# Kernel optimization log

Hardware: AMD Instinct MI355X
Metric: run time of the kernel (lower is better)

## Reference

```python
import jax, jax.numpy as jnp
import numpy as np
from math import log2, ceil

HEADS = 16
BLOCK = 16
EPS = 1e-8


def flip_every_two(t):
    # flip adjacent pairs along axis 1: (B, n, ...) with n even
    B, n = t.shape[0], t.shape[1]
    rest = t.shape[2:]
    t = t.reshape(B, n // 2, 2, *rest)
    t = jnp.flip(t, axis=2)
    return t.reshape(B, n, *rest)


def masked_aggregate(t, mask, average=True):
    # t: (B, n, 2, d), mask: (B, n, 2) bool; aggregate over axis=2
    m = mask[..., None]
    s = jnp.where(m, t, 0.0).sum(axis=2)
    total = mask.sum(axis=2)  # (B, n) int
    if average:
        s = s / jnp.clip(total, 1)[..., None].astype(t.dtype)
    return jnp.where((total == 0)[..., None], 0.0, s)


def _forward(x, Wq, bq, Wk, bk, Wv, bv, mask):
    b, n, hidden = x.shape
    h, bsz, d = HEADS, BLOCK, hidden // HEADS
    scale = d ** -0.5
    pad_to_len = 2 ** ceil(log2(n))
    pad = pad_to_len - n
    if pad != 0:
        x = jnp.pad(x, ((0, 0), (0, pad), (0, 0)))
        mask = jnp.pad(mask, ((0, 0), (0, pad)), constant_values=False)
    N = pad_to_len

    def split_heads(t):  # (b, N, h*d) -> (b*h, N, d)
        return t.reshape(b, N, h, d).transpose(0, 2, 1, 3).reshape(b * h, N, d)

    q = split_heads(x @ Wq + bq) * scale
    k = split_heads(x @ Wk + bk)
    v = split_heads(x @ Wv + bv)
    m = jnp.broadcast_to(mask[:, None, :], (b, h, N)).reshape(b * h, N)

    num_levels = int(log2(N // bsz)) - 2
    qkvs = [(q, k, v, m)]
    for _ in range(num_levels):
        B, L, _ = q.shape
        q2 = q.reshape(B, L // 2, 2, d)
        k2 = k.reshape(B, L // 2, 2, d)
        v2 = v.reshape(B, L // 2, 2, d)
        m2 = m.reshape(B, L // 2, 2)
        q = masked_aggregate(q2, m2, average=True)
        k = masked_aggregate(k2, m2, average=True)
        v = masked_aggregate(v2, m2, average=False)
        m = jnp.any(m2, axis=2)
        qkvs.append((q, k, v, m))
    qkvs = [qkvs[0]] + qkvs

    Ys = []
    for ind, (ql, kl, vl, ml) in enumerate(reversed(qkvs)):
        is_last = ind == len(qkvs) - 1
        B, L, _ = ql.shape
        nb = L // bsz
        qb = ql.reshape(B, nb, bsz, d)
        kb = kl.reshape(B, nb, bsz, d)
        vb = vl.reshape(B, nb, bsz, d)
        mb = ml.reshape(B, nb, bsz)
        k_mask = mb if is_last else flip_every_two(mb)
        S_mask = mb[..., :, None] & k_mask[..., None, :]  # (B, nb, bsz, bsz)
        if not is_last:
            kb = flip_every_two(kb)
            vb = flip_every_two(vb)
        S = jnp.einsum('bnid,bnjd->bnij', qb, kb)
        S = jnp.where(S_mask, S, jnp.finfo(S.dtype).min)
        S = S - S.max(axis=-1, keepdims=True)
        A = jnp.exp(S)
        Y = jnp.einsum('bnij,bnjd->bnid', A, vb)
        Ys.append((Y.reshape(B, L, d), A.sum(axis=-1).reshape(B, L)))

    Y, A = Ys[0]
    for ind in range(1, len(Ys)):
        is_last = ind == len(Ys) - 1
        if not is_last:
            Y = jnp.repeat(Y, 2, axis=1)
            A = jnp.repeat(A, 2, axis=1)
        Y = Ys[ind][0] + Y
        A = Ys[ind][1] + A

    out = Y / (A + EPS)[..., None]  # (b*h, N, d)
    out = out.reshape(b, h, N, d).transpose(0, 2, 1, 3).reshape(b, N, hidden)
    return out[:, :n]


def setup_inputs():
    key = jax.random.key(0)
    ks = jax.random.split(key, 7)
    b, n, hidden = 2, 8192, 1024
    s = 1.0 / np.sqrt(hidden)
    x = jax.random.normal(ks[0], (b, n, hidden), jnp.float32)
    mask = jnp.ones((b, n), dtype=bool)
    Wq = jax.random.normal(ks[1], (hidden, hidden), jnp.float32) * s
    Wk = jax.random.normal(ks[2], (hidden, hidden), jnp.float32) * s
    Wv = jax.random.normal(ks[3], (hidden, hidden), jnp.float32) * s
    bq = jax.random.normal(ks[4], (hidden,), jnp.float32) * 0.01
    bk = jax.random.normal(ks[5], (hidden,), jnp.float32) * 0.01
    bv = jax.random.normal(ks[6], (hidden,), jnp.float32) * 0.01
    return {"x": x, "mask": mask, "Wq": Wq, "bq": bq, "Wk": Wk, "bk": bk, "Wv": Wv, "bv": bv}


def reference(x, mask, Wq, bq, Wk, bk, Wv, bv):
    return _forward(x, Wq, bq, Wk, bk, Wv, bv, mask)
```

## Files before the change

### kernel.cpp

```cpp
#include <hip/hip_runtime.h>
#include <hip/hip_bf16.h>

typedef __attribute__((ext_vector_type(4))) float f32x4;
typedef __attribute__((ext_vector_type(8))) __bf16 bf16x8;
typedef __attribute__((ext_vector_type(4))) unsigned int u32x4;

#define TE 33423360ull

__device__ __forceinline__ unsigned short f2b_rne(float f) {
  unsigned u = __float_as_uint(f);
  return (unsigned short)((u + 0x7fffu + ((u >> 16) & 1u)) >> 16);
}
__device__ __forceinline__ float b2f(unsigned s) { return __uint_as_float(s << 16); }

__device__ __forceinline__ void gload_lds16(const unsigned short* g, unsigned short* l) {
  __builtin_amdgcn_global_load_lds((const __attribute__((address_space(1))) void*)g,
                                   (__attribute__((address_space(3))) void*)l, 16, 0, 0);
}

__global__ void conv_x(const float* __restrict__ x, unsigned short* __restrict__ xb) {
  size_t i = ((size_t)blockIdx.x * 256 + threadIdx.x) * 8;
  f32x4 A = *(const f32x4*)(x + i);
  f32x4 B = *(const f32x4*)(x + i + 4);
  u32x4 o;
  o[0] = f2b_rne(A[0]) | ((unsigned)f2b_rne(A[1]) << 16);
  o[1] = f2b_rne(A[2]) | ((unsigned)f2b_rne(A[3]) << 16);
  o[2] = f2b_rne(B[0]) | ((unsigned)f2b_rne(B[1]) << 16);
  o[3] = f2b_rne(B[2]) | ((unsigned)f2b_rne(B[3]) << 16);
  *(u32x4*)(xb + i) = o;
}

__global__ void transpose_w(const float* __restrict__ Wq, const float* __restrict__ Wk,
                            const float* __restrict__ Wv, unsigned short* __restrict__ wt) {
  int z = blockIdx.z;
  const float* W = (z == 0) ? Wq : (z == 1) ? Wk : Wv;
  __shared__ float t[32][33];
  int n0 = blockIdx.x * 32, k0 = blockIdx.y * 32;
  int tx = threadIdx.x, ty = threadIdx.y;
#pragma unroll
  for (int j = 0; j < 4; ++j)
    t[ty + j * 8][tx] = W[(size_t)(k0 + ty + j * 8) * 1024 + n0 + tx];
  __syncthreads();
  unsigned short* o = wt + (size_t)z * 1048576;
#pragma unroll
  for (int j = 0; j < 4; ++j)
    o[(size_t)(n0 + ty + j * 8) * 1024 + k0 + tx] = f2b_rne(t[tx][ty + j * 8]);
}

__global__ __launch_bounds__(256) void gemm_qkv(
    const unsigned short* __restrict__ xb, const unsigned short* __restrict__ wt,
    const float* __restrict__ bq, const float* __restrict__ bk, const float* __restrict__ bv,
    unsigned short* __restrict__ qkv) {
  int z = blockIdx.z;
  const unsigned short* w = wt + (size_t)z * 1048576;
  int flat = blockIdx.y * 8 + blockIdx.x;
  int swz = (flat & 7) * 128 + (flat >> 3);
  int m0 = (swz >> 3) * 128, n0 = (swz & 7) * 128;
  __shared__ unsigned short At[8192];
  __shared__ unsigned short Bt[8192];
  int tid = threadIdx.x;
  int lane = tid & 63, wid = tid >> 6;
  int g = lane >> 4, r16 = lane & 15;
  int wm = (wid >> 1) * 64, wn = (wid & 1) * 64;
  int srow = wid * 8 + (lane >> 3);
  int scol = ((lane & 7) ^ (lane >> 3)) * 8;
  f32x4 zero4 = {0.f, 0.f, 0.f, 0.f};
  f32x4 acc[4][4];
#pragma unroll
  for (int i = 0; i < 4; ++i)
#pragma unroll
    for (int j = 0; j < 4; ++j) acc[i][j] = zero4;

  for (int kt = 0; kt < 16; ++kt) {
#pragma unroll
    for (int c = 0; c < 4; ++c) {
      const unsigned short* ga = xb + (size_t)(m0 + c * 32 + srow) * 1024 + kt * 64 + scol;
      gload_lds16(ga, At + c * 2048 + wid * 512);
    }
#pragma unroll
    for (int c = 0; c < 4; ++c) {
      const unsigned short* gb = w + (size_t)(n0 + c * 32 + srow) * 1024 + kt * 64 + scol;
      gload_lds16(gb, Bt + c * 2048 + wid * 512);
    }
    __syncthreads();
#pragma unroll
    for (int kk = 0; kk < 2; ++kk) {
      bf16x8 af[4], bf_[4];
#pragma unroll
      for (int t = 0; t < 4; ++t) {
        int m = wm + t * 16 + r16;
        af[t] = *(const bf16x8*)((const char*)At + m * 128 + (((kk * 4 + g) ^ (m & 7)) * 16));
        int n = wn + t * 16 + r16;
        bf_[t] = *(const bf16x8*)((const char*)Bt + n * 128 + (((kk * 4 + g) ^ (n & 7)) * 16));
      }
#pragma unroll
      for (int i = 0; i < 4; ++i)
#pragma unroll
        for (int j = 0; j < 4; ++j)
          acc[i][j] = __builtin_amdgcn_mfma_f32_16x16x32_bf16(af[i], bf_[j], acc[i][j], 0, 0, 0);
    }
    __syncthreads();
  }
  const float* bias = (z == 0) ? bq : (z == 1) ? bk : bv;
  float scale = (z == 0) ? 0.125f : 1.0f;
  unsigned short* outp = qkv + (size_t)z * TE;
#pragma unroll
  for (int i = 0; i < 4; ++i) {
#pragma unroll
    for (int j = 0; j < 4; ++j) {
      int col = n0 + wn + j * 16 + r16;
      float bc = bias[col];
#pragma unroll
      for (int r = 0; r < 4; ++r) {
        int row = m0 + wm + i * 16 + g * 4 + r;
        float val = (acc[i][j][r] + bc) * scale;
        int bh = ((row >> 13) << 4) + (col >> 6);
        int pos = row & 8191;
        int dd = col & 63;
        outp[((size_t)bh * 8192 + pos) * 64 + dd] = f2b_rne(val);
      }
    }
  }
}

__global__ __launch_bounds__(256) void agg_all(unsigned short* __restrict__ qkv) {
  int seg = blockIdx.x, bh = blockIdx.y, z = blockIdx.z;
  unsigned short* tb = qkv + (size_t)z * TE;
  __shared__ unsigned short b0[16384];
  __shared__ unsigned short b1[8192];
  int t = threadIdx.x;
  const unsigned short* ip = tb + ((size_t)bh * 8192 + (size_t)seg * 256) * 64;
#pragma unroll
  for (int j = 0; j < 8; ++j)
    *(u32x4*)(b0 + (j * 256 + t) * 8) = *(const u32x4*)(ip + (size_t)(j * 256 + t) * 8);
  __syncthreads();
  float sc = (z < 2) ? 0.5f : 1.0f;
  long off = 8192;
  unsigned short* src = b0;
  unsigned short* dst = b1;
  for (int l = 1; l <= 7; ++l) {
    int R = 256 >> l;
    int chunks = R * 32;
    for (int c = t; c < chunks; c += 256) {
      int r = c >> 5, cc = c & 31;
      unsigned a = *(const unsigned*)(src + (2 * r) * 64 + cc * 2);
      unsigned b = *(const unsigned*)(src + (2 * r + 1) * 64 + cc * 2);
      float lo = (b2f(a & 0xffffu) + b2f(b & 0xffffu)) * sc;
      float hi = (b2f(a >> 16) + b2f(b >> 16)) * sc;
      unsigned o = f2b_rne(lo) | ((unsigned)f2b_rne(hi) << 16);
      *(unsigned*)(dst + r * 64 + cc * 2) = o;
      unsigned short* op =
          tb + (size_t)off * 2048 + ((size_t)bh * (8192 >> l) + (size_t)seg * R + r) * 64;
      *(unsigned*)(op + cc * 2) = o;
    }
    __syncthreads();
    off += 8192 >> l;
    unsigned short* tmp = src; src = dst; dst = tmp;
  }
}

union U8 { bf16x8 v; unsigned short u[8]; };

__device__ __forceinline__ void attn_unit(
    const unsigned short* kb, const unsigned short* vb, bf16x8 qf0, bf16x8 qf1,
    int g, int qr, f32x4 (&acc)[4], float& aacc) {
  bf16x8 kf0 = *(const bf16x8*)(kb + qr * 64 + g * 8);
  bf16x8 kf1 = *(const bf16x8*)(kb + qr * 64 + 32 + g * 8);
  f32x4 s = {0.f, 0.f, 0.f, 0.f};
  s = __builtin_amdgcn_mfma_f32_16x16x32_bf16(kf0, qf0, s, 0, 0, 0);
  s = __builtin_amdgcn_mfma_f32_16x16x32_bf16(kf1, qf1, s, 0, 0, 0);
  float mx = fmaxf(fmaxf(s[0], s[1]), fmaxf(s[2], s[3]));
  mx = fmaxf(mx, __shfl_xor(mx, 16));
  mx = fmaxf(mx, __shfl_xor(mx, 32));
  float av[4], asum = 0.f;
#pragma unroll
  for (int r = 0; r < 4; ++r) { av[r] = __expf(s[r] - mx); asum += av[r]; }
  asum += __shfl_xor(asum, 16);
  asum += __shfl_xor(asum, 32);
  aacc += asum;
  U8 A_;
#pragma unroll
  for (int r = 0; r < 4; ++r) A_.u[r] = f2b_rne(av[r]);
#pragma unroll
  for (int r = 4; r < 8; ++r) A_.u[r] = 0;
#pragma unroll
  for (int cg = 0; cg < 4; ++cg) {
    int c = cg * 16 + qr;
    U8 B_;
#pragma unroll
    for (int r = 0; r < 4; ++r) B_.u[r] = vb[(g * 4 + r) * 64 + c];
#pragma unroll
    for (int r = 4; r < 8; ++r) B_.u[r] = 0;
    acc[cg] = __builtin_amdgcn_mfma_f32_16x16x32_bf16(A_.v, B_.v, acc[cg], 0, 0, 0);
  }
}

__global__ __launch_bounds__(64) void attn_fused(const unsigned short* __restrict__ qkv,
                                                 float* __restrict__ outp) {
  int flat = blockIdx.y * 512 + blockIdx.x;
  int fb = (flat & 7) * 2048 + (flat >> 3);
  int bh = fb >> 9, B0 = fb & 511;
  int lane = threadIdx.x;
  int g = lane >> 4, qr = lane & 15;
  const unsigned short* qt = qkv;
  const unsigned short* kt = qkv + TE;
  const unsigned short* vt = qkv + 2 * TE;
  f32x4 acc[4];
#pragma unroll
  for (int cg = 0; cg < 4; ++cg) acc[cg] = (f32x4){0.f, 0.f, 0.f, 0.f};
  float aacc = 0.f;
  int off = 0;
#pragma unroll
  for (int l = 0; l <= 7; ++l) {
    int L = 8192 >> l;
    size_t base = (size_t)off * 2048 + (size_t)bh * L * 64;
    const unsigned short* qb = qt + base;
    const unsigned short* kb = kt + base;
    const unsigned short* vb = vt + base;
    int qrow = (B0 * 16 + qr) >> l;
    bf16x8 qf0 = *(const bf16x8*)(qb + (size_t)qrow * 64 + g * 8);
    bf16x8 qf1 = *(const bf16x8*)(qb + (size_t)qrow * 64 + 32 + g * 8);
    int P = B0 >> l;
    if (l == 0) {
      attn_unit(kb + (size_t)P * 1024, vb + (size_t)P * 1024, qf0, qf1, g, qr, acc, aacc);
      attn_unit(kb + (size_t)(P ^ 1) * 1024, vb + (size_t)(P ^ 1) * 1024, qf0, qf1, g, qr, acc, aacc);
    } else {
      int S_ = P ^ 1;
      attn_unit(kb + (size_t)S_ * 1024, vb + (size_t)S_ * 1024, qf0, qf1, g, qr, acc, aacc);
    }
    off += L;
  }
  int b_ = bh >> 4, h_ = bh & 15;
#pragma unroll
  for (int r = 0; r < 4; ++r) {
    int p = g * 4 + r;
    float ap = __shfl(aacc, p);
    float inv = 1.0f / (ap + 1e-8f);
    float* od = outp + ((size_t)(b_ * 8192 + B0 * 16 + p)) * 1024 + h_ * 64 + qr;
#pragma unroll
    for (int cg = 0; cg < 4; ++cg) od[cg * 16] = acc[cg][r] * inv;
  }
}

extern "C" void kernel_launch(void* const* d_in, const int* in_sizes, int n_in,
                              void* d_out, int out_size, void* d_ws, size_t ws_size,
                              hipStream_t stream) {
  const float* x = (const float*)d_in[0];
  const float* Wq = (const float*)d_in[2];
  const float* bq = (const float*)d_in[3];
  const float* Wk = (const float*)d_in[4];
  const float* bk = (const float*)d_in[5];
  const float* Wv = (const float*)d_in[6];
  const float* bv = (const float*)d_in[7];
  float* out = (float*)d_out;

  char* ws = (char*)d_ws;
  size_t o = 0;
  unsigned short* qkv = (unsigned short*)(ws + o); o += 200540160ull;
  unsigned short* wt = (unsigned short*)(ws + o); o += 6291456ull;
  unsigned short* xb = (unsigned short*)(ws + o); o += 33554432ull;
  if (ws_size < o) return;

  conv_x<<<8192, 256, 0, stream>>>(x, xb);
  transpose_w<<<dim3(32, 32, 3), dim3(32, 8), 0, stream>>>(Wq, Wk, Wv, wt);
  gemm_qkv<<<dim3(8, 128, 3), 256, 0, stream>>>(xb, wt, bq, bk, bv, qkv);
  agg_all<<<dim3(32, 32, 3), 256, 0, stream>>>(qkv);
  attn_fused<<<dim3(512, 32), 64, 0, stream>>>(qkv, out);
}
```

Before: 259.6 us.

## Double-buffer QKV GEMM LDS tiles and stage epilogue through LDS for vector stores

Splits the GEMM's shared memory into two buffers so the next K-tile's global-to-LDS loads are issued before computing on the current tile, overlapping memory latency with MFMA work. The epilogue now writes bf16 results into a padded LDS tile and then emits 16-byte vectorized row stores to the head-split output layout, replacing scattered 2-byte stores. This doubles LDS usage (64KB per block), which may reduce occupancy.

```diff
diff --git a/kernel.cpp b/kernel.cpp
--- a/kernel.cpp
+++ b/kernel.cpp
@@ -56,14 +56,26 @@
   int flat = blockIdx.y * 8 + blockIdx.x;
   int swz = (flat & 7) * 128 + (flat >> 3);
   int m0 = (swz >> 3) * 128, n0 = (swz & 7) * 128;
-  __shared__ unsigned short At[8192];
-  __shared__ unsigned short Bt[8192];
+  __shared__ unsigned short lds[32768];
   int tid = threadIdx.x;
   int lane = tid & 63, wid = tid >> 6;
   int g = lane >> 4, r16 = lane & 15;
   int wm = (wid >> 1) * 64, wn = (wid & 1) * 64;
   int srow = wid * 8 + (lane >> 3);
   int scol = ((lane & 7) ^ (lane >> 3)) * 8;
+
+  auto stage = [&](int b, int kt) {
+    unsigned short* Ab = lds + b * 16384;
+    unsigned short* Bb = Ab + 8192;
+#pragma unroll
+    for (int c = 0; c < 4; ++c) {
+      gload_lds16(xb + (size_t)(m0 + c * 32 + srow) * 1024 + kt * 64 + scol,
+                  Ab + c * 2048 + wid * 512);
+      gload_lds16(w + (size_t)(n0 + c * 32 + srow) * 1024 + kt * 64 + scol,
+                  Bb + c * 2048 + wid * 512);
+    }
+  };
+
   f32x4 zero4 = {0.f, 0.f, 0.f, 0.f};
   f32x4 acc[4][4];
 #pragma unroll
@@ -71,27 +83,22 @@
 #pragma unroll
     for (int j = 0; j < 4; ++j) acc[i][j] = zero4;
 
+  stage(0, 0);
+  __syncthreads();
   for (int kt = 0; kt < 16; ++kt) {
-#pragma unroll
-    for (int c = 0; c < 4; ++c) {
-      const unsigned short* ga = xb + (size_t)(m0 + c * 32 + srow) * 1024 + kt * 64 + scol;
-      gload_lds16(ga, At + c * 2048 + wid * 512);
-    }
-#pragma unroll
-    for (int c = 0; c < 4; ++c) {
-      const unsigned short* gb = w + (size_t)(n0 + c * 32 + srow) * 1024 + kt * 64 + scol;
-      gload_lds16(gb, Bt + c * 2048 + wid * 512);
-    }
-    __syncthreads();
+    int cb = kt & 1;
+    if (kt < 15) stage(cb ^ 1, kt + 1);
+    const char* Ab = (const char*)(lds + cb * 16384);
+    const char* Bb = Ab + 16384;
 #pragma unroll
     for (int kk = 0; kk < 2; ++kk) {
       bf16x8 af[4], bf_[4];
 #pragma unroll
       for (int t = 0; t < 4; ++t) {
         int m = wm + t * 16 + r16;
-        af[t] = *(const bf16x8*)((const char*)At + m * 128 + (((kk * 4 + g) ^ (m & 7)) * 16));
+        af[t] = *(const bf16x8*)(Ab + m * 128 + (((kk * 4 + g) ^ (m & 7)) * 16));
         int n = wn + t * 16 + r16;
-        bf_[t] = *(const bf16x8*)((const char*)Bt + n * 128 + (((kk * 4 + g) ^ (n & 7)) * 16));
+        bf_[t] = *(const bf16x8*)(Bb + n * 128 + (((kk * 4 + g) ^ (n & 7)) * 16));
       }
 #pragma unroll
       for (int i = 0; i < 4; ++i)
@@ -101,26 +108,31 @@
     }
     __syncthreads();
   }
+
   const float* bias = (z == 0) ? bq : (z == 1) ? bk : bv;
   float scale = (z == 0) ? 0.125f : 1.0f;
-  unsigned short* outp = qkv + (size_t)z * TE;
+  unsigned short* Ct = lds;
 #pragma unroll
   for (int i = 0; i < 4; ++i) {
 #pragma unroll
     for (int j = 0; j < 4; ++j) {
-      int col = n0 + wn + j * 16 + r16;
-      float bc = bias[col];
+      int col = wn + j * 16 + r16;
+      float bc = bias[n0 + col];
 #pragma unroll
       for (int r = 0; r < 4; ++r) {
-        int row = m0 + wm + i * 16 + g * 4 + r;
-        float val = (acc[i][j][r] + bc) * scale;
-        int bh = ((row >> 13) << 4) + (col >> 6);
-        int pos = row & 8191;
-        int dd = col & 63;
-        outp[((size_t)bh * 8192 + pos) * 64 + dd] = f2b_rne(val);
+        int row = wm + i * 16 + g * 4 + r;
+        Ct[row * 136 + col] = f2b_rne((acc[i][j][r] + bc) * scale);
       }
     }
   }
+  __syncthreads();
+  int rr = tid >> 1, hc = (tid & 1) * 64;
+  int R = m0 + rr, Cb = n0 + hc;
+  int bh = ((R >> 13) << 4) + (Cb >> 6);
+  unsigned short* outp = qkv + (size_t)z * TE + ((size_t)bh * 8192 + (size_t)(R & 8191)) * 64;
+#pragma unroll
+  for (int ch = 0; ch < 8; ++ch)
+    *(u32x4*)(outp + ch * 8) = *(const u32x4*)(Ct + rr * 136 + hc + ch * 8);
 }
 
 __global__ __launch_bounds__(256) void agg_all(unsigned short* __restrict__ qkv) {
```

Result: no change. 258.7 us (-0.3%).
